# Performance work log

Hardware: AMD Instinct MI355X
Metric: run time of the kernel (lower is better)

Reference implementation:

```python
import jax, jax.numpy as jnp
import numpy as np

N, E, DIN, H, H1, H2, B, DEC = 20000, 320000, 128, 4, 64, 32, 4096, 512


def _seg_softmax(e, seg, n):
    # numerically stable softmax over edges grouped by destination node
    m = jax.ops.segment_max(e, seg, num_segments=n)
    p = jnp.exp(e - m[seg])
    s = jax.ops.segment_sum(p, seg, num_segments=n)
    return p / (s[seg] + 1e-16)


def _prelu(x, a):
    return jnp.where(x >= 0, x, a * x)


def _gat(x, src, dst, n, w, a_src, a_dst, b, concat):
    # PyG GATConv: shared linear, additive attention, leaky_relu(0.2), softmax per dst
    h_, c = a_src.shape
    h = (x @ w).reshape(-1, h_, c)                      # [n, H, C]
    al = jnp.einsum('nhc,hc->nh', h, a_src)[src] + jnp.einsum('nhc,hc->nh', h, a_dst)[dst]
    alpha = _seg_softmax(jax.nn.leaky_relu(al, 0.2), dst, n)  # [e, H]
    out = jax.ops.segment_sum(alpha[..., None] * h[src], dst, num_segments=n)
    out = out.reshape(n, h_ * c) if concat else out.mean(1)
    return out + b


def _gt(x, src, dst, n, wq, bq, wk, bk, wv, bv, ws, bs, heads, concat):
    # PyG TransformerConv: scaled dot-product attention over edges + root skip
    c = wq.shape[1] // heads
    q = (x @ wq + bq).reshape(-1, heads, c)
    k = (x @ wk + bk).reshape(-1, heads, c)
    v = (x @ wv + bv).reshape(-1, heads, c)
    e = (q[dst] * k[src]).sum(-1) / jnp.sqrt(jnp.float32(c))  # [e, heads]
    alpha = _seg_softmax(e, dst, n)
    agg = jax.ops.segment_sum(alpha[..., None] * v[src], dst, num_segments=n)
    agg = agg.reshape(n, heads * c) if concat else agg.mean(1)
    return agg + x @ ws + bs


def _forward(fl, edge_index, idx):
    (x_o, x_a, gat1_w, gat1_asrc, gat1_adst, gat1_b, gat2_w, gat2_asrc, gat2_adst, gat2_b,
     pg1, pg2, gt1_wq, gt1_bq, gt1_wk, gt1_bk, gt1_wv, gt1_bv, gt1_ws, gt1_bs,
     gt2_wq, gt2_bq, gt2_wk, gt2_bk, gt2_wv, gt2_bv, gt2_ws, gt2_bs, pt1, pt2,
     fuse_w, fuse_b, mlp1_w, mlp1_b, disc_w, disc_b,
     fus_w1, fus_b1, fus_w2, fus_b2, fus_w3, fus_b3, adv_w, adv_b) = fl
    n = x_o.shape[0]
    src, dst = edge_index[0], edge_index[1]
    # GATConv adds self loops by default; TransformerConv does not
    loop = jnp.arange(n, dtype=src.dtype)
    src_g = jnp.concatenate([src, loop])
    dst_g = jnp.concatenate([dst, loop])

    def branch_gat(x):
        x1 = _prelu(_gat(x, src_g, dst_g, n, gat1_w, gat1_asrc, gat1_adst, gat1_b, True), pg1)
        return _prelu(_gat(x1, src_g, dst_g, n, gat2_w, gat2_asrc, gat2_adst, gat2_b, False), pg2)

    def branch_gt(x):
        x1 = _prelu(_gt(x, src, dst, n, gt1_wq, gt1_bq, gt1_wk, gt1_bk, gt1_wv, gt1_bv, gt1_ws, gt1_bs, H, True), pt1)
        return _prelu(_gt(x1, src, dst, n, gt2_wq, gt2_bq, gt2_wk, gt2_bk, gt2_wv, gt2_bv, gt2_ws, gt2_bs, 1, False), pt2)

    x2_o = jnp.concatenate([branch_gat(x_o), branch_gt(x_o)], 1) @ fuse_w + fuse_b
    x2_a = jnp.concatenate([branch_gat(x_a), branch_gt(x_a)], 1) @ fuse_w + fuse_b

    def summary(z):
        return jax.nn.sigmoid(z.mean(0)) @ mlp1_w + mlp1_b   # [H2]

    h_os, h_os_a = summary(x2_o), summary(x2_a)

    def disc(cvec, hp, hm):
        # Bilinear(n_h, n_h, 1): sc = h W c^T + b
        s1 = (hp @ disc_w) @ cvec + disc_b[0]
        s2 = (hm @ disc_w) @ cvec + disc_b[0]
        return jnp.stack([s1, s2], 1)                       # [N, 2]

    ret_os = disc(h_os, x2_o, x2_a)
    ret_os_a = disc(h_os_a, x2_a, x2_o)

    # default task_type: direct indexing of node embeddings
    hcat = jnp.concatenate([x2_o[idx[0]], x2_o[idx[1]]], 1)  # [B, 2*H2]
    hh = jax.nn.relu(hcat @ fus_w1 + fus_b1)
    log = hh @ fus_w2 + fus_b2
    log1 = hh @ fus_w3 + fus_b3

    sc1 = (x2_o @ adv_w + adv_b).sum(1)[None, :]
    sc2 = (x2_a @ adv_w + adv_b).sum(1)[None, :]
    logits = jnp.concatenate([sc1, sc2], 1)                  # [1, 2N]
    return (log, ret_os, ret_os_a, x2_o, logits, log1)


_SHAPES = {
    'x_o': (N, DIN), 'x_a': (N, DIN),
    'gat1_w': (DIN, H * H1), 'gat1_asrc': (H, H1), 'gat1_adst': (H, H1), 'gat1_b': (H * H1,),
    'gat2_w': (H * H1, H2), 'gat2_asrc': (1, H2), 'gat2_adst': (1, H2), 'gat2_b': (H2,),
    'pg1': (H * H1,), 'pg2': (H2,),
    'gt1_wq': (DIN, H * H1), 'gt1_bq': (H * H1,), 'gt1_wk': (DIN, H * H1), 'gt1_bk': (H * H1,),
    'gt1_wv': (DIN, H * H1), 'gt1_bv': (H * H1,), 'gt1_ws': (DIN, H * H1), 'gt1_bs': (H * H1,),
    'gt2_wq': (H * H1, H2), 'gt2_bq': (H2,), 'gt2_wk': (H * H1, H2), 'gt2_bk': (H2,),
    'gt2_wv': (H * H1, H2), 'gt2_bv': (H2,), 'gt2_ws': (H * H1, H2), 'gt2_bs': (H2,),
    'pt1': (H * H1,), 'pt2': (H2,),
    'fuse_w': (2 * H2, H2), 'fuse_b': (H2,),
    'mlp1_w': (H2, H2), 'mlp1_b': (H2,),
    'disc_w': (H2, H2), 'disc_b': (1,),
    'fus_w1': (2 * H2, DEC), 'fus_b1': (DEC,), 'fus_w2': (DEC, 2), 'fus_b2': (2,),
    'fus_w3': (DEC, 2), 'fus_b3': (2,),
    'adv_w': (H2, H2), 'adv_b': (H2,),
}


def setup_inputs() -> dict:
    key = jax.random.key(0)
    inp = {}
    for i, (name, shp) in enumerate(_SHAPES.items()):
        inp[name] = jax.random.normal(jax.random.fold_in(key, i), shp, jnp.float32) * 0.05
    inp['edge_index'] = jax.random.randint(jax.random.fold_in(key, 100), (2, E), 0, N, dtype=jnp.int32)
    inp['idx'] = jax.random.randint(jax.random.fold_in(key, 101), (2, B), 0, N, dtype=jnp.int32)
    return inp


def reference(x_o, x_a, gat1_w, gat1_asrc, gat1_adst, gat1_b, gat2_w, gat2_asrc, gat2_adst, gat2_b,
              pg1, pg2, gt1_wq, gt1_bq, gt1_wk, gt1_bk, gt1_wv, gt1_bv, gt1_ws, gt1_bs,
              gt2_wq, gt2_bq, gt2_wk, gt2_bk, gt2_wv, gt2_bv, gt2_ws, gt2_bs, pt1, pt2,
              fuse_w, fuse_b, mlp1_w, mlp1_b, disc_w, disc_b,
              fus_w1, fus_b1, fus_w2, fus_b2, fus_w3, fus_b3, adv_w, adv_b,
              edge_index, idx):
    fl = (x_o, x_a, gat1_w, gat1_asrc, gat1_adst, gat1_b, gat2_w, gat2_asrc, gat2_adst, gat2_b,
          pg1, pg2, gt1_wq, gt1_bq, gt1_wk, gt1_bk, gt1_wv, gt1_bv, gt1_ws, gt1_bs,
          gt2_wq, gt2_bq, gt2_wk, gt2_bk, gt2_wv, gt2_bv, gt2_ws, gt2_bs, pt1, pt2,
          fuse_w, fuse_b, mlp1_w, mlp1_b, disc_w, disc_b,
          fus_w1, fus_b1, fus_w2, fus_b2, fus_w3, fus_b3, adv_w, adv_b)
    return _forward(fl, edge_index, idx)
```

## Files before the change

### kernel.cpp

```cpp
#include <hip/hip_runtime.h>
#include <math.h>

#define NN 20000
#define NE 320000
#define NB 4096

typedef unsigned short u16;
typedef unsigned char u8;
typedef __attribute__((ext_vector_type(8))) short short8;
typedef __attribute__((ext_vector_type(4))) float f32x4;
typedef __attribute__((ext_vector_type(2))) float f32x2;

#define FP8_SCALE 16.0f
#define FP8_INV 0.0625f
#define LOG2E 1.44269504088896341f

__device__ __forceinline__ float b2f(u16 u) {
  unsigned int x = ((unsigned int)u) << 16;
  return __uint_as_float(x);
}
__device__ __forceinline__ u16 f2b(float f) {
  unsigned int x = __float_as_uint(f);
  return (u16)((x + 0x7fffu + ((x >> 16) & 1u)) >> 16);
}
__device__ __forceinline__ float q2f(u8 b) {
  f32x2 v = __builtin_amdgcn_cvt_pk_f32_fp8((int)b, false);
  return v[0];
}
__device__ __forceinline__ void q4(unsigned int u, float* f) {
  f32x2 lo = __builtin_amdgcn_cvt_pk_f32_fp8((int)u, false);
  f32x2 hi = __builtin_amdgcn_cvt_pk_f32_fp8((int)u, true);
  f[0] = lo[0]; f[1] = lo[1]; f[2] = hi[0]; f[3] = hi[1];
}
template <int CTRL>
__device__ __forceinline__ float dppadd(float x) {
  int y = __builtin_amdgcn_update_dpp(0, __float_as_int(x), CTRL, 0xf, 0xf, true);
  return x + __int_as_float(y);
}
__device__ __forceinline__ float red16(float x) {
  x = dppadd<0xB1>(x);
  x = dppadd<0x4E>(x);
  x = dppadd<0x124>(x);
  x = dppadd<0x128>(x);
  return x;
}


__global__ void k_pack1(const float* __restrict__ w0, const float* __restrict__ w1,
                        const float* __restrict__ w2, const float* __restrict__ w3,
                        const float* __restrict__ w4, const float* __restrict__ b1,
                        const float* __restrict__ b2, const float* __restrict__ b3,
                        const float* __restrict__ b4, u16* __restrict__ Wt,
                        float* __restrict__ bp) {
  int t = blockIdx.x * blockDim.x + threadIdx.x;
  if (t < 1280 * 128) {
    int j = t >> 7, k = t & 127;
    int seg = j >> 8, jj = j & 255;
    const float* s = (seg == 0) ? w0 : (seg == 1) ? w1 : (seg == 2) ? w2 : (seg == 3) ? w3 : w4;
    Wt[t] = f2b(s[k * 256 + jj]);
  }
  if (t < 1280) {
    int seg = t >> 8, jj = t & 255;
    bp[t] = (seg == 0) ? 0.0f : (seg == 1) ? b1[jj] : (seg == 2) ? b2[jj] : (seg == 3) ? b3[jj] : b4[jj];
  }
}

__global__ void k_pack2(const float* __restrict__ wq, const float* __restrict__ wk,
                        const float* __restrict__ wv, const float* __restrict__ ws,
                        const float* __restrict__ wg, const float* __restrict__ bq,
                        const float* __restrict__ bk, const float* __restrict__ bv,
                        const float* __restrict__ bs, u16* __restrict__ Wt,
                        float* __restrict__ bp) {
  int t = blockIdx.x * blockDim.x + threadIdx.x;
  if (t < 160 * 256) {
    int j = t >> 8, k = t & 255;
    int seg = j >> 5, jj = j & 31;
    const float* s = (seg == 0) ? wq : (seg == 1) ? wk : (seg == 2) ? wv : (seg == 3) ? ws : wg;
    Wt[t] = f2b(s[k * 32 + jj]);
  }
  if (t < 160) {
    int seg = t >> 5, jj = t & 31;
    bp[t] = (seg == 0) ? bq[jj] : (seg == 1) ? bk[jj] : (seg == 2) ? bv[jj] : (seg == 3) ? bs[jj] : 0.0f;
  }
}

__global__ void k_tobf16x2(const float* __restrict__ xo, const float* __restrict__ xa,
                           u16* __restrict__ bo, u16* __restrict__ ba) {
  int t = blockIdx.x * blockDim.x + threadIdx.x;
  if (t >= 2 * NN * 128) return;
  if (t < NN * 128) bo[t] = f2b(xo[t]);
  else ba[t - NN * 128] = f2b(xa[t - NN * 128]);
}


__global__ void k_hist(const int* __restrict__ dst, int* __restrict__ deg) {
  int t = blockIdx.x * blockDim.x + threadIdx.x;
  if (t < NE) atomicAdd(&deg[dst[t]], 1);
}

__global__ void k_scan20000(const int* __restrict__ deg, int* __restrict__ offs,
                            int* __restrict__ cur) {
  __shared__ int part[1024];
  int t = threadIdx.x;
  int loc[20];
  int s = 0;
#pragma unroll
  for (int i = 0; i < 20; ++i) {
    int idx = t * 20 + i;
    int v = (idx < NN) ? deg[idx] : 0;
    loc[i] = s;
    s += v;
  }
  part[t] = s;
  __syncthreads();
  for (int off = 1; off < 1024; off <<= 1) {
    int v = (t >= off) ? part[t - off] : 0;
    __syncthreads();
    part[t] += v;
    __syncthreads();
  }
  int base = (t > 0) ? part[t - 1] : 0;
#pragma unroll
  for (int i = 0; i < 20; ++i) {
    int idx = t * 20 + i;
    if (idx < NN) {
      offs[idx] = base + loc[i];
      cur[idx] = base + loc[i];
    }
  }
  if (t == 1023) offs[NN] = part[1023];
}

__global__ void k_scatter(const int* __restrict__ src, const int* __restrict__ dst,
                          int* __restrict__ cur, int* __restrict__ esrcs) {
  int t = blockIdx.x * blockDim.x + threadIdx.x;
  if (t >= NE) return;
  int d = dst[t];
  int pos = atomicAdd(&cur[d], 1);
  esrcs[pos] = src[t];
}


template <int LAYER>
__global__ void k_mfma_gemm_s(const u16* __restrict__ A0, const u16* __restrict__ A1,
                              int asel, const u16* __restrict__ Bt,
                              const float* __restrict__ bias, int M, int K, int Nc,
                              u8* __restrict__ G, u16* __restrict__ Cb) {
  const u16* A = (blockIdx.x >= (unsigned)asel) ? A1 : A0;
  int m0 = blockIdx.y * 128, n0 = blockIdx.x * 128;
  int wid = threadIdx.x >> 6, lane = threadIdx.x & 63;
  int mw = m0 + (wid & 1) * 64, nw = n0 + (wid >> 1) * 64;
  int arow = mw + (lane & 15);
  int bcol = nw + (lane & 15);
  int kblk = (lane >> 4) * 8;
  f32x4 acc[4][4] = {};
  const short8 zero8 = {0, 0, 0, 0, 0, 0, 0, 0};
  for (int k0 = 0; k0 < K; k0 += 32) {
    short8 af[4], bf[4];
#pragma unroll
    for (int mf = 0; mf < 4; ++mf) {
      int r = arow + mf * 16;
      if (r > M - 1) r = M - 1;
      af[mf] = *reinterpret_cast<const short8*>(&A[(size_t)r * K + k0 + kblk]);
    }
#pragma unroll
    for (int nf = 0; nf < 4; ++nf) {
      int c = bcol + nf * 16;
      bf[nf] = (c < Nc) ? *reinterpret_cast<const short8*>(&Bt[(size_t)c * K + k0 + kblk])
                        : zero8;
    }
#pragma unroll
    for (int mf = 0; mf < 4; ++mf)
#pragma unroll
      for (int nf = 0; nf < 4; ++nf)
        acc[mf][nf] = __builtin_amdgcn_mfma_f32_16x16x32_bf16(bf[nf], af[mf],
                                                              acc[mf][nf], 0, 0, 0);
  }
  const int CSTR = (LAYER == 1) ? 512 : 64;
  const int GSTR = (LAYER == 1) ? 768 : 96;
#pragma unroll
  for (int mf = 0; mf < 4; ++mf) {
    int row = mw + mf * 16 + (lane & 15);
    if (row >= M) continue;
#pragma unroll
    for (int nf = 0; nf < 4; ++nf) {
      int col0 = nw + nf * 16 + ((lane >> 4) << 2);
      if (col0 >= Nc) continue;
      float4 bs4 = *reinterpret_cast<const float4*>(&bias[col0]);
      float v0 = acc[mf][nf][0] + bs4.x;
      float v1 = acc[mf][nf][1] + bs4.y;
      float v2 = acc[mf][nf][2] + bs4.z;
      float v3 = acc[mf][nf][3] + bs4.w;
      int seg = (LAYER == 1) ? (col0 >> 8) : (col0 >> 5);
      bool tobf = (LAYER == 1) ? (seg == 1 || seg == 4) : (seg == 0 || seg == 3);
      if (tobf) {
        int ccol = (LAYER == 1) ? ((seg == 1) ? col0 - 256 : col0 - 768)
                                : ((seg == 0) ? col0 : col0 - 64);
        ushort4 w4;
        w4.x = f2b(v0); w4.y = f2b(v1); w4.z = f2b(v2); w4.w = f2b(v3);
        *reinterpret_cast<ushort4*>(&Cb[(size_t)row * CSTR + ccol]) = w4;
      } else {
        int gcol = (LAYER == 1) ? ((seg == 0) ? col0 : col0 - 256)
                                : ((seg == 4) ? col0 - 64 : col0 - 32);
        unsigned int p = (unsigned int)__builtin_amdgcn_cvt_pk_fp8_f32(
            v0 * FP8_SCALE, v1 * FP8_SCALE, 0, false);
        p = (unsigned int)__builtin_amdgcn_cvt_pk_fp8_f32(
            v2 * FP8_SCALE, v3 * FP8_SCALE, (int)p, true);
        *reinterpret_cast<unsigned int*>(&G[(size_t)row * GSTR + gcol]) = p;
      }
    }
  }
}


__global__ void k_gat_al8(const u8* __restrict__ h, int stride, int coff,
                          const float* __restrict__ asrc, const float* __restrict__ adst,
                          float* __restrict__ als, float* __restrict__ ald, int total,
                          int heads, int c) {
  int i = blockIdx.x * blockDim.x + threadIdx.x;
  if (i >= total) return;
  int node = i / heads, hd = i - node * heads;
  const u8* hp = h + (size_t)node * stride + coff + hd * c;
  const float* as = asrc + hd * c;
  const float* ad = adst + hd * c;
  float s1 = 0.0f, s2 = 0.0f;
  for (int k = 0; k < c; k += 4) {
    float f[4];
    q4(*reinterpret_cast<const unsigned int*>(&hp[k]), f);
#pragma unroll
    for (int j = 0; j < 4; ++j) {
      s1 = fmaf(f[j], as[k + j], s1);
      s2 = fmaf(f[j], ad[k + j], s2);
    }
  }
  als[i] = s1 * (FP8_INV * LOG2E);
  ald[i] = s2 * (FP8_INV * LOG2E);
}

__global__ void k_agg256_fused(const int* __restrict__ offs, const int* __restrict__ esrcs,
                               const float* __restrict__ als, const float* __restrict__ ald,
                               const u8* __restrict__ G8, const u16* __restrict__ C1b,
                               const float* __restrict__ gbias,
                               const float* __restrict__ pg, const float* __restrict__ pt,
                               u16* __restrict__ outG, u16* __restrict__ outT) {
  __shared__ float part[2][64][10];
  int g = threadIdx.x >> 6;
  int dl = g >> 1, half = g & 1;
  int d = blockIdx.x * 2 + dl;
  int lane = threadIdx.x & 63;
  int head = lane >> 4, c4 = lane << 2;
  ushort4 q4v = *reinterpret_cast<const ushort4*>(&C1b[(size_t)d * 512 + c4]);
  float q0 = b2f(q4v.x), q1 = b2f(q4v.y), q2 = b2f(q4v.z), q3 = b2f(q4v.w);
  float aldd = ald[d * 4 + head];
  float ga0 = 0, ga1 = 0, ga2 = 0, ga3 = 0, gden = 0.0f;
  float ta0 = 0, ta1 = 0, ta2 = 0, ta3 = 0;
  float tden = half ? 0.0f : 1e-16f;
  int bs = offs[d] + half, be = offs[d + 1];
  const float GTC = 0.125f * FP8_INV * LOG2E;
  unsigned int f0 = 0, k0 = 0, v0 = 0, f1 = 0, k1 = 0, v1 = 0;
  float al0 = 0.0f, al1 = 0.0f;
  if (bs < be) {
    int s = esrcs[bs];
    const u8* row = &G8[(size_t)s * 768];
    f0 = *reinterpret_cast<const unsigned int*>(&row[c4]);
    k0 = *reinterpret_cast<const unsigned int*>(&row[256 + c4]);
    v0 = *reinterpret_cast<const unsigned int*>(&row[512 + c4]);
    al0 = als[s * 4 + head];
  }
  if (bs + 2 < be) {
    int s = esrcs[bs + 2];
    const u8* row = &G8[(size_t)s * 768];
    f1 = *reinterpret_cast<const unsigned int*>(&row[c4]);
    k1 = *reinterpret_cast<const unsigned int*>(&row[256 + c4]);
    v1 = *reinterpret_cast<const unsigned int*>(&row[512 + c4]);
    al1 = als[s * 4 + head];
  }
  for (int i = bs; i < be; i += 2) {
    unsigned int f2_ = 0, k2_ = 0, v2_ = 0;
    float al2_ = 0.0f;
    if (i + 4 < be) {
      int s = esrcs[i + 4];
      const u8* row = &G8[(size_t)s * 768];
      f2_ = *reinterpret_cast<const unsigned int*>(&row[c4]);
      k2_ = *reinterpret_cast<const unsigned int*>(&row[256 + c4]);
      v2_ = *reinterpret_cast<const unsigned int*>(&row[512 + c4]);
      al2_ = als[s * 4 + head];
    }
    float kf[4];
    q4(k0, kf);
    float pp = q0 * kf[0];
    pp = fmaf(q1, kf[1], pp);
    pp = fmaf(q2, kf[2], pp);
    pp = fmaf(q3, kf[3], pp);
    pp = red16(pp);
    float pet = exp2f(pp * GTC);
    float v = al0 + aldd;
    float peg = exp2f(v >= 0.0f ? v : 0.2f * v);
    float ff[4], vf[4];
    q4(f0, ff);
    q4(v0, vf);
    ga0 = fmaf(peg, ff[0], ga0);
    ga1 = fmaf(peg, ff[1], ga1);
    ga2 = fmaf(peg, ff[2], ga2);
    ga3 = fmaf(peg, ff[3], ga3);
    gden += peg;
    ta0 = fmaf(pet, vf[0], ta0);
    ta1 = fmaf(pet, vf[1], ta1);
    ta2 = fmaf(pet, vf[2], ta2);
    ta3 = fmaf(pet, vf[3], ta3);
    tden += pet;
    f0 = f1; k0 = k1; v0 = v1; al0 = al1;
    f1 = f2_; k1 = k2_; v1 = v2_; al1 = al2_;
  }
  if (half == 0) {
    float v = als[d * 4 + head] + aldd;
    float pe = exp2f(v >= 0.0f ? v : 0.2f * v);
    float ff[4];
    q4(*reinterpret_cast<const unsigned int*>(&G8[(size_t)d * 768 + c4]), ff);
    ga0 = fmaf(pe, ff[0], ga0);
    ga1 = fmaf(pe, ff[1], ga1);
    ga2 = fmaf(pe, ff[2], ga2);
    ga3 = fmaf(pe, ff[3], ga3);
    gden += pe;
  }
  if (half == 1) {
    float* p = part[dl][lane];
    p[0] = ga0; p[1] = ga1; p[2] = ga2; p[3] = ga3; p[4] = gden;
    p[5] = ta0; p[6] = ta1; p[7] = ta2; p[8] = ta3; p[9] = tden;
  }
  __syncthreads();
  if (half == 1) return;
  const float* p = part[dl][lane];
  ga0 += p[0]; ga1 += p[1]; ga2 += p[2]; ga3 += p[3]; gden += p[4];
  ta0 += p[5]; ta1 += p[6]; ta2 += p[7]; ta3 += p[8]; tden += p[9];
  float ig = FP8_INV / gden, it = FP8_INV / tden;
  float o0 = ga0 * ig + gbias[c4 + 0];
  float o1 = ga1 * ig + gbias[c4 + 1];
  float o2 = ga2 * ig + gbias[c4 + 2];
  float o3 = ga3 * ig + gbias[c4 + 3];
  o0 = o0 >= 0.0f ? o0 : pg[c4 + 0] * o0;
  o1 = o1 >= 0.0f ? o1 : pg[c4 + 1] * o1;
  o2 = o2 >= 0.0f ? o2 : pg[c4 + 2] * o2;
  o3 = o3 >= 0.0f ? o3 : pg[c4 + 3] * o3;
  ushort4 wg4;
  wg4.x = f2b(o0); wg4.y = f2b(o1); wg4.z = f2b(o2); wg4.w = f2b(o3);
  *reinterpret_cast<ushort4*>(&outG[(size_t)d * 256 + c4]) = wg4;
  ushort4 sk = *reinterpret_cast<const ushort4*>(&C1b[(size_t)d * 512 + 256 + c4]);
  float u0 = ta0 * it + b2f(sk.x);
  float u1 = ta1 * it + b2f(sk.y);
  float u2 = ta2 * it + b2f(sk.z);
  float u3 = ta3 * it + b2f(sk.w);
  u0 = u0 >= 0.0f ? u0 : pt[c4 + 0] * u0;
  u1 = u1 >= 0.0f ? u1 : pt[c4 + 1] * u1;
  u2 = u2 >= 0.0f ? u2 : pt[c4 + 2] * u2;
  u3 = u3 >= 0.0f ? u3 : pt[c4 + 3] * u3;
  ushort4 wt4;
  wt4.x = f2b(u0); wt4.y = f2b(u1); wt4.z = f2b(u2); wt4.w = f2b(u3);
  *reinterpret_cast<ushort4*>(&outT[(size_t)d * 256 + c4]) = wt4;
}

__global__ void k_agg32_fuse(const int* __restrict__ offs, const int* __restrict__ esrcs,
                             const float* __restrict__ als, const float* __restrict__ ald,
                             const u8* __restrict__ G28, const u16* __restrict__ C2b,
                             const float* __restrict__ gbias,
                             const float* __restrict__ pg, const float* __restrict__ pt,
                             const float* __restrict__ fw, const float* __restrict__ fb,
                             float* __restrict__ x2out, float* __restrict__ colsum) {
  __shared__ float xgv[8][32], xtv[8][32];
  int g = threadIdx.x >> 5, l = threadIdx.x & 31;
  int d = blockIdx.x * 8 + g;
  float qv = b2f(C2b[(size_t)d * 64 + l]);
  float aldd = ald[d];
  float ga = 0.0f, gden = 0.0f;
  float ta = 0.0f, tden = 1e-16f;
  int b0 = offs[d], b1 = offs[d + 1];
  const float GTC2 = 0.17677669529663687f * FP8_INV * LOG2E;
  u8 kc = 0, vc = 0, hc = 0;
  float alc = 0;
  if (b0 < b1) {
    int sc = esrcs[b0];
    const u8* row = &G28[(size_t)sc * 96];
    kc = row[l]; vc = row[32 + l]; hc = row[64 + l];
    alc = als[sc];
  }
  for (int i = b0; i < b1; ++i) {
    u8 kn = kc, vn = vc, hn = hc;
    float aln = alc;
    if (i + 1 < b1) {
      int sn = esrcs[i + 1];
      const u8* row = &G28[(size_t)sn * 96];
      kn = row[l]; vn = row[32 + l]; hn = row[64 + l];
      aln = als[sn];
    }
    float pp = qv * q2f(kc);
    pp = red16(pp);
    pp += __shfl_xor(pp, 16, 32);
    float pet = exp2f(pp * GTC2);
    float v = alc + aldd;
    float peg = exp2f(v >= 0.0f ? v : 0.2f * v);
    ga = fmaf(peg, q2f(hc), ga);
    gden += peg;
    ta = fmaf(pet, q2f(vc), ta);
    tden += pet;
    kc = kn; vc = vn; hc = hn; alc = aln;
  }
  {
    float v = als[d] + aldd;
    float pe = exp2f(v >= 0.0f ? v : 0.2f * v);
    ga = fmaf(pe, q2f(G28[(size_t)d * 96 + 64 + l]), ga);
    gden += pe;
  }
  float og = ga * FP8_INV / gden + gbias[l];
  og = og >= 0.0f ? og : pg[l] * og;
  float ot = ta * FP8_INV / tden + b2f(C2b[(size_t)d * 64 + 32 + l]);
  ot = ot >= 0.0f ? ot : pt[l] * ot;
  xgv[g][l] = og;
  xtv[g][l] = ot;
  __syncthreads();
  float acc = fb[l];
#pragma unroll
  for (int i = 0; i < 32; ++i) {
    acc = fmaf(xgv[g][i], fw[i * 32 + l], acc);
    acc = fmaf(xtv[g][i], fw[(32 + i) * 32 + l], acc);
  }
  x2out[(size_t)d * 32 + l] = acc;
  __syncthreads();
  xgv[g][l] = acc;
  __syncthreads();
  if (g == 0) {
    float s = acc;
#pragma unroll
    for (int i = 1; i < 8; ++i) s += xgv[i][l];
    atomicAdd(&colsum[(blockIdx.x & 7) * 32 + l], s);
  }
}


__global__ void k_disc_all(const float* __restrict__ x2o, const float* __restrict__ x2a_,
                           const float* __restrict__ cso, const float* __restrict__ csa,
                           const float* __restrict__ mlp_w, const float* __restrict__ mlp_b,
                           const float* __restrict__ disc_w, const float* __restrict__ db,
                           const float* __restrict__ aw, const float* __restrict__ ab,
                           float* __restrict__ ret_os, float* __restrict__ ret_os_a,
                           float* __restrict__ logits) {
  __shared__ float sgv[64], h1s[32], h2s[32], m1[32], m2[32], sadv[33];
  int t = threadIdx.x;
  if (t < 64) {
    int j = t & 31;
    const float* cs = (t < 32) ? cso : csa;
    float m = 0.0f;
#pragma unroll
    for (int i = 0; i < 8; ++i) m += cs[i * 32 + j];
    sgv[t] = 1.0f / (1.0f + expf(-m / (float)NN));
  }
  if (t >= 64 && t < 96) {
    int j = t & 31;
    float s = 0.0f;
#pragma unroll
    for (int i = 0; i < 32; ++i) s += aw[j * 32 + i];
    sadv[j] = s;
  } else if (t == 96) {
    float s = 0.0f;
#pragma unroll
    for (int i = 0; i < 32; ++i) s += ab[i];
    sadv[32] = s;
  }
  __syncthreads();
  if (t < 64) {
    int j = t & 31;
    const float* sg = (t < 32) ? sgv : sgv + 32;
    float acc = mlp_b[j];
#pragma unroll
    for (int i = 0; i < 32; ++i) acc = fmaf(sg[i], mlp_w[i * 32 + j], acc);
    (t < 32 ? h1s : h2s)[j] = acc;
  }
  __syncthreads();
  if (t < 64) {
    int k = t & 31;
    const float* hv = (t < 32) ? h1s : h2s;
    float acc = 0.0f;
#pragma unroll
    for (int i = 0; i < 32; ++i) acc = fmaf(disc_w[k * 32 + i], hv[i], acc);
    (t < 32 ? m1 : m2)[k] = acc;
  }
  __syncthreads();
  int n = blockIdx.x * blockDim.x + t;
  if (n >= NN) return;
  const float* a = x2o + (size_t)n * 32;
  const float* b = x2a_ + (size_t)n * 32;
  float s_oo = 0, s_ao = 0, s_aa = 0, s_oa = 0;
  float lo = sadv[32], la = sadv[32];
#pragma unroll
  for (int i = 0; i < 32; ++i) {
    float v1 = m1[i], v2 = m2[i], av = sadv[i];
    float ai = a[i], bi = b[i];
    s_oo = fmaf(ai, v1, s_oo);
    s_ao = fmaf(bi, v1, s_ao);
    s_aa = fmaf(bi, v2, s_aa);
    s_oa = fmaf(ai, v2, s_oa);
    lo = fmaf(ai, av, lo);
    la = fmaf(bi, av, la);
  }
  float bb = db[0];
  ret_os[n * 2 + 0] = s_oo + bb;
  ret_os[n * 2 + 1] = s_ao + bb;
  ret_os_a[n * 2 + 0] = s_aa + bb;
  ret_os_a[n * 2 + 1] = s_oa + bb;
  logits[n] = lo;
  logits[NN + n] = la;
}

__global__ void k_dec(const float* __restrict__ x2o, const int* __restrict__ idx0,
                      const int* __restrict__ idx1, const float* __restrict__ w1,
                      const float* __restrict__ b1, const float* __restrict__ w2,
                      const float* __restrict__ b2, const float* __restrict__ w3,
                      const float* __restrict__ b3, float* __restrict__ logo,
                      float* __restrict__ log1) {
  __shared__ float hhs[512];
  int bb = blockIdx.x;
  const float* r0 = x2o + (size_t)idx0[bb] * 32;
  const float* r1 = x2o + (size_t)idx1[bb] * 32;
  int t = threadIdx.x;
  for (int n = t; n < 512; n += 256) {
    float acc = b1[n];
#pragma unroll
    for (int i = 0; i < 32; ++i) {
      acc = fmaf(r0[i], w1[i * 512 + n], acc);
      acc = fmaf(r1[i], w1[(32 + i) * 512 + n], acc);
    }
    hhs[n] = fmaxf(acc, 0.0f);
  }
  __syncthreads();
  int g = t >> 6, lane = t & 63;
  const float* ws = (g < 2) ? w2 : w3;
  int jj = g & 1;
  float acc = 0.0f;
#pragma unroll
  for (int k = 0; k < 8; ++k) acc = fmaf(hhs[lane + k * 64], ws[(lane + k * 64) * 2 + jj], acc);
  acc += __shfl_xor(acc, 32);
  acc += __shfl_xor(acc, 16);
  acc += __shfl_xor(acc, 8);
  acc += __shfl_xor(acc, 4);
  acc += __shfl_xor(acc, 2);
  acc += __shfl_xor(acc, 1);
  if (lane == 0) {
    float b = (g < 2) ? b2[jj] : b3[jj];
    ((g < 2) ? logo : log1)[bb * 2 + jj] = acc + b;
  }
}


extern "C" void kernel_launch(void* const* d_in, const int* in_sizes, int n_in,
                              void* d_out, int out_size, void* d_ws, size_t ws_size,
                              hipStream_t stream) {
  const float* x_o = (const float*)d_in[0];
  const float* x_a = (const float*)d_in[1];
  const float* gat1_w = (const float*)d_in[2];
  const float* gat1_asrc = (const float*)d_in[3];
  const float* gat1_adst = (const float*)d_in[4];
  const float* gat1_b = (const float*)d_in[5];
  const float* gat2_w = (const float*)d_in[6];
  const float* gat2_asrc = (const float*)d_in[7];
  const float* gat2_adst = (const float*)d_in[8];
  const float* gat2_b = (const float*)d_in[9];
  const float* pg1 = (const float*)d_in[10];
  const float* pg2 = (const float*)d_in[11];
  const float* gt1_wq = (const float*)d_in[12];
  const float* gt1_bq = (const float*)d_in[13];
  const float* gt1_wk = (const float*)d_in[14];
  const float* gt1_bk = (const float*)d_in[15];
  const float* gt1_wv = (const float*)d_in[16];
  const float* gt1_bv = (const float*)d_in[17];
  const float* gt1_ws = (const float*)d_in[18];
  const float* gt1_bs = (const float*)d_in[19];
  const float* gt2_wq = (const float*)d_in[20];
  const float* gt2_bq = (const float*)d_in[21];
  const float* gt2_wk = (const float*)d_in[22];
  const float* gt2_bk = (const float*)d_in[23];
  const float* gt2_wv = (const float*)d_in[24];
  const float* gt2_bv = (const float*)d_in[25];
  const float* gt2_ws = (const float*)d_in[26];
  const float* gt2_bs = (const float*)d_in[27];
  const float* pt1 = (const float*)d_in[28];
  const float* pt2 = (const float*)d_in[29];
  const float* fuse_w = (const float*)d_in[30];
  const float* fuse_b = (const float*)d_in[31];
  const float* mlp1_w = (const float*)d_in[32];
  const float* mlp1_b = (const float*)d_in[33];
  const float* disc_w = (const float*)d_in[34];
  const float* disc_b = (const float*)d_in[35];
  const float* fus_w1 = (const float*)d_in[36];
  const float* fus_b1 = (const float*)d_in[37];
  const float* fus_w2 = (const float*)d_in[38];
  const float* fus_b2 = (const float*)d_in[39];
  const float* fus_w3 = (const float*)d_in[40];
  const float* fus_b3 = (const float*)d_in[41];
  const float* adv_w = (const float*)d_in[42];
  const float* adv_b = (const float*)d_in[43];
  const int* ei = (const int*)d_in[44];
  const int* idxp = (const int*)d_in[45];
  const int* esrc = ei;
  const int* edst = ei + NE;
  const int* idx0 = idxp;
  const int* idx1 = idxp + NB;

  float* w = (float*)d_ws;
  size_t o = 0;
  u8* G8 = (u8*)(w + o); o += 3840000;
  u16* C1b = (u16*)(w + o); o += 5120000;
  u8* G28 = (u8*)(w + o); o += 480000;
  u16* C2b = (u16*)(w + o); o += 640000;
  u16* bufB = (u16*)(w + o); o += 2560000;
  u16* bufE = (u16*)(w + o); o += 2560000;
  u16* xb_o = (u16*)(w + o); o += 1280000;
  u16* xb_a = (u16*)(w + o); o += 1280000;
  u16* Wt1 = (u16*)(w + o); o += 81920;
  u16* Wt2 = (u16*)(w + o); o += 20480;
  float* bp1 = w + o; o += 1280;
  float* bp2 = w + o; o += 160;
  float* als = w + o; o += NN * 4;
  float* ald = w + o; o += NN * 4;
  float* x2a = w + o; o += NN * 32;
  int* deg = (int*)(w + o); o += NN;
  int* offs = (int*)(w + o); o += NN + 8;
  int* cur = (int*)(w + o); o += NN;
  int* esrcs = (int*)(w + o); o += NE;
  float* colsum_o = w + o; o += 256;
  float* colsum_a = w + o; o += 256;

  float* out = (float*)d_out;
  float* out_log = out;
  float* out_ret = out + 8192;
  float* out_reta = out + 48192;
  float* out_x2o = out + 88192;
  float* out_logit = out + 728192;
  float* out_log1 = out + 768192;

  k_pack1<<<(1280 * 128 + 255) / 256, 256, 0, stream>>>(gat1_w, gt1_wq, gt1_wk, gt1_wv,
                                                        gt1_ws, gt1_bq, gt1_bk, gt1_bv,
                                                        gt1_bs, Wt1, bp1);
  k_pack2<<<(160 * 256 + 255) / 256, 256, 0, stream>>>(gt2_wq, gt2_wk, gt2_wv, gt2_ws,
                                                       gat2_w, gt2_bq, gt2_bk, gt2_bv,
                                                       gt2_bs, Wt2, bp2);
  k_tobf16x2<<<(2 * NN * 128 + 255) / 256, 256, 0, stream>>>(x_o, x_a, xb_o, xb_a);
  hipMemsetAsync(deg, 0, NN * sizeof(int), stream);
  hipMemsetAsync(colsum_o, 0, 512 * sizeof(float), stream);
  k_hist<<<(NE + 255) / 256, 256, 0, stream>>>(edst, deg);
  k_scan20000<<<1, 1024, 0, stream>>>(deg, offs, cur);
  k_scatter<<<(NE + 255) / 256, 256, 0, stream>>>(esrc, edst, cur, esrcs);

  auto branch = [&](const u16* xb, float* x2out, float* colsum) {
    {
      dim3 g(10, (NN + 127) / 128);
      k_mfma_gemm_s<1><<<g, 256, 0, stream>>>(xb, xb, 999, Wt1, bp1, NN, 128, 1280,
                                              G8, C1b);
    }
    k_gat_al8<<<(NN * 4 + 255) / 256, 256, 0, stream>>>(G8, 768, 0, gat1_asrc, gat1_adst,
                                                        als, ald, NN * 4, 4, 64);
    k_agg256_fused<<<NN / 2, 256, 0, stream>>>(offs, esrcs, als, ald, G8, C1b,
                                               gat1_b, pg1, pt1, bufB, bufE);
    {
      dim3 g(2, (NN + 127) / 128);
      k_mfma_gemm_s<2><<<g, 256, 0, stream>>>(bufE, bufB, 1, Wt2, bp2, NN, 256, 160,
                                              G28, C2b);
    }
    k_gat_al8<<<(NN + 255) / 256, 256, 0, stream>>>(G28, 96, 64, gat2_asrc, gat2_adst,
                                                    als, ald, NN, 1, 32);
    k_agg32_fuse<<<NN / 8, 256, 0, stream>>>(offs, esrcs, als, ald, G28, C2b,
                                             gat2_b, pg2, pt2, fuse_w, fuse_b,
                                             x2out, colsum);
  };

  branch(xb_o, out_x2o, colsum_o);
  branch(xb_a, x2a, colsum_a);

  k_disc_all<<<(NN + 255) / 256, 256, 0, stream>>>(out_x2o, x2a, colsum_o, colsum_a,
                                                   mlp1_w, mlp1_b, disc_w, disc_b,
                                                   adv_w, adv_b, out_ret, out_reta,
                                                   out_logit);
  k_dec<<<NB, 256, 0, stream>>>(out_x2o, idx0, idx1, fus_w1, fus_b1, fus_w2, fus_b2,
                                fus_w3, fus_b3, out_log, out_log1);
}
```

Before: 446.8 us.

## Fuse bf16 input conversion and GAT attention logits into GEMM epilogue

Removes the separate fp32-to-bf16 conversion kernel by having the layer-1 GEMM load fp32 inputs and convert them in registers. It also drops both k_gat_al8 launches and computes the per-head source and destination attention logits inside the GEMM epilogue, using full-precision accumulators and cross-lane shuffles. This saves four kernel launches and the global round trips for the bf16 copies and fp8 reloads. In exchange, the GEMM reads twice as many input bytes and converts redundantly across column blocks. The logits now come from unquantized values rather than fp8 values, which slightly changes numerics.

```diff
diff --git a/kernel.cpp b/kernel.cpp
--- a/kernel.cpp
+++ b/kernel.cpp
@@ -43,6 +43,20 @@
   x = dppadd<0x124>(x);
   x = dppadd<0x128>(x);
   return x;
+}
+
+__device__ __forceinline__ short8 lda8(const u16* p) {
+  return *reinterpret_cast<const short8*>(p);
+}
+__device__ __forceinline__ short8 lda8(const float* p) {
+  float4 a = *reinterpret_cast<const float4*>(p);
+  float4 b = *reinterpret_cast<const float4*>(p + 4);
+  short8 r;
+  r[0] = (short)f2b(a.x); r[1] = (short)f2b(a.y);
+  r[2] = (short)f2b(a.z); r[3] = (short)f2b(a.w);
+  r[4] = (short)f2b(b.x); r[5] = (short)f2b(b.y);
+  r[6] = (short)f2b(b.z); r[7] = (short)f2b(b.w);
+  return r;
 }
 
 
@@ -84,14 +98,6 @@
   }
 }
 
-__global__ void k_tobf16x2(const float* __restrict__ xo, const float* __restrict__ xa,
-                           u16* __restrict__ bo, u16* __restrict__ ba) {
-  int t = blockIdx.x * blockDim.x + threadIdx.x;
-  if (t >= 2 * NN * 128) return;
-  if (t < NN * 128) bo[t] = f2b(xo[t]);
-  else ba[t - NN * 128] = f2b(xa[t - NN * 128]);
-}
-
 
 __global__ void k_hist(const int* __restrict__ dst, int* __restrict__ deg) {
   int t = blockIdx.x * blockDim.x + threadIdx.x;
@@ -141,12 +147,15 @@
 }
 
 
-template <int LAYER>
-__global__ void k_mfma_gemm_s(const u16* __restrict__ A0, const u16* __restrict__ A1,
+template <int LAYER, typename TA>
+__global__ void k_mfma_gemm_s(const TA* __restrict__ A0, const TA* __restrict__ A1,
                               int asel, const u16* __restrict__ Bt,
                               const float* __restrict__ bias, int M, int K, int Nc,
-                              u8* __restrict__ G, u16* __restrict__ Cb) {
-  const u16* A = (blockIdx.x >= (unsigned)asel) ? A1 : A0;
+                              u8* __restrict__ G, u16* __restrict__ Cb,
+                              const float* __restrict__ gasrc,
+                              const float* __restrict__ gadst,
+                              float* __restrict__ als, float* __restrict__ ald) {
+  const TA* A = (blockIdx.x >= (unsigned)asel) ? A1 : A0;
   int m0 = blockIdx.y * 128, n0 = blockIdx.x * 128;
   int wid = threadIdx.x >> 6, lane = threadIdx.x & 63;
   int mw = m0 + (wid & 1) * 64, nw = n0 + (wid >> 1) * 64;
@@ -161,7 +170,7 @@
     for (int mf = 0; mf < 4; ++mf) {
       int r = arow + mf * 16;
       if (r > M - 1) r = M - 1;
-      af[mf] = *reinterpret_cast<const short8*>(&A[(size_t)r * K + k0 + kblk]);
+      af[mf] = lda8(&A[(size_t)r * K + k0 + kblk]);
     }
 #pragma unroll
     for (int nf = 0; nf < 4; ++nf) {
@@ -178,10 +187,12 @@
   }
   const int CSTR = (LAYER == 1) ? 512 : 64;
   const int GSTR = (LAYER == 1) ? 768 : 96;
+  bool alwave = (LAYER == 1) ? (n0 < 256) : (nw == 128);
 #pragma unroll
   for (int mf = 0; mf < 4; ++mf) {
     int row = mw + mf * 16 + (lane & 15);
-    if (row >= M) continue;
+    bool rv = row < M;
+    float alsum = 0.0f, aldsum = 0.0f;
 #pragma unroll
     for (int nf = 0; nf < 4; ++nf) {
       int col0 = nw + nf * 16 + ((lane >> 4) << 2);
@@ -191,6 +202,19 @@
       float v1 = acc[mf][nf][1] + bs4.y;
       float v2 = acc[mf][nf][2] + bs4.z;
       float v3 = acc[mf][nf][3] + bs4.w;
+      if (alwave) {
+        if (LAYER == 1) {
+          alsum += v0 * gasrc[col0] + v1 * gasrc[col0 + 1] + v2 * gasrc[col0 + 2] +
+                   v3 * gasrc[col0 + 3];
+          aldsum += v0 * gadst[col0] + v1 * gadst[col0 + 1] + v2 * gadst[col0 + 2] +
+                    v3 * gadst[col0 + 3];
+        } else if (col0 >= 128 && col0 < 160) {
+          int c = col0 - 128;
+          alsum += v0 * gasrc[c] + v1 * gasrc[c + 1] + v2 * gasrc[c + 2] + v3 * gasrc[c + 3];
+          aldsum += v0 * gadst[c] + v1 * gadst[c + 1] + v2 * gadst[c + 2] + v3 * gadst[c + 3];
+        }
+      }
+      if (!rv) continue;
       int seg = (LAYER == 1) ? (col0 >> 8) : (col0 >> 5);
       bool tobf = (LAYER == 1) ? (seg == 1 || seg == 4) : (seg == 0 || seg == 3);
       if (tobf) {
@@ -209,33 +233,25 @@
         *reinterpret_cast<unsigned int*>(&G[(size_t)row * GSTR + gcol]) = p;
       }
     }
-  }
-}
-
-
-__global__ void k_gat_al8(const u8* __restrict__ h, int stride, int coff,
-                          const float* __restrict__ asrc, const float* __restrict__ adst,
-                          float* __restrict__ als, float* __restrict__ ald, int total,
-                          int heads, int c) {
-  int i = blockIdx.x * blockDim.x + threadIdx.x;
-  if (i >= total) return;
-  int node = i / heads, hd = i - node * heads;
-  const u8* hp = h + (size_t)node * stride + coff + hd * c;
-  const float* as = asrc + hd * c;
-  const float* ad = adst + hd * c;
-  float s1 = 0.0f, s2 = 0.0f;
-  for (int k = 0; k < c; k += 4) {
-    float f[4];
-    q4(*reinterpret_cast<const unsigned int*>(&hp[k]), f);
-#pragma unroll
-    for (int j = 0; j < 4; ++j) {
-      s1 = fmaf(f[j], as[k + j], s1);
-      s2 = fmaf(f[j], ad[k + j], s2);
-    }
-  }
-  als[i] = s1 * (FP8_INV * LOG2E);
-  ald[i] = s2 * (FP8_INV * LOG2E);
-}
+    if (alwave) {
+      alsum += __shfl_xor(alsum, 16);
+      alsum += __shfl_xor(alsum, 32);
+      aldsum += __shfl_xor(aldsum, 16);
+      aldsum += __shfl_xor(aldsum, 32);
+      if (lane < 16 && rv) {
+        if (LAYER == 1) {
+          int head = nw >> 6;
+          als[row * 4 + head] = alsum * LOG2E;
+          ald[row * 4 + head] = aldsum * LOG2E;
+        } else {
+          als[row] = alsum * LOG2E;
+          ald[row] = aldsum * LOG2E;
+        }
+      }
+    }
+  }
+}
+
 
 __global__ void k_agg256_fused(const int* __restrict__ offs, const int* __restrict__ esrcs,
                                const float* __restrict__ als, const float* __restrict__ ald,
@@ -612,8 +628,6 @@
   u16* C2b = (u16*)(w + o); o += 640000;
   u16* bufB = (u16*)(w + o); o += 2560000;
   u16* bufE = (u16*)(w + o); o += 2560000;
-  u16* xb_o = (u16*)(w + o); o += 1280000;
-  u16* xb_a = (u16*)(w + o); o += 1280000;
   u16* Wt1 = (u16*)(w + o); o += 81920;
   u16* Wt2 = (u16*)(w + o); o += 20480;
   float* bp1 = w + o; o += 1280;
@@ -642,37 +656,34 @@
   k_pack2<<<(160 * 256 + 255) / 256, 256, 0, stream>>>(gt2_wq, gt2_wk, gt2_wv, gt2_ws,
                                                        gat2_w, gt2_bq, gt2_bk, gt2_bv,
                                                        gt2_bs, Wt2, bp2);
-  k_tobf16x2<<<(2 * NN * 128 + 255) / 256, 256, 0, stream>>>(x_o, x_a, xb_o, xb_a);
   hipMemsetAsync(deg, 0, NN * sizeof(int), stream);
   hipMemsetAsync(colsum_o, 0, 512 * sizeof(float), stream);
   k_hist<<<(NE + 255) / 256, 256, 0, stream>>>(edst, deg);
   k_scan20000<<<1, 1024, 0, stream>>>(deg, offs, cur);
   k_scatter<<<(NE + 255) / 256, 256, 0, stream>>>(esrc, edst, cur, esrcs);
 
-  auto branch = [&](const u16* xb, float* x2out, float* colsum) {
+  auto branch = [&](const float* x, float* x2out, float* colsum) {
     {
       dim3 g(10, (NN + 127) / 128);
-      k_mfma_gemm_s<1><<<g, 256, 0, stream>>>(xb, xb, 999, Wt1, bp1, NN, 128, 1280,
-                                              G8, C1b);
-    }
-    k_gat_al8<<<(NN * 4 + 255) / 256, 256, 0, stream>>>(G8, 768, 0, gat1_asrc, gat1_adst,
-                                                        als, ald, NN * 4, 4, 64);
+      k_mfma_gemm_s<1, float><<<g, 256, 0, stream>>>(x, x, 999, Wt1, bp1, NN, 128, 1280,
+                                                     G8, C1b, gat1_asrc, gat1_adst,
+                                                     als, ald);
+    }
     k_agg256_fused<<<NN / 2, 256, 0, stream>>>(offs, esrcs, als, ald, G8, C1b,
                                                gat1_b, pg1, pt1, bufB, bufE);
     {
       dim3 g(2, (NN + 127) / 128);
-      k_mfma_gemm_s<2><<<g, 256, 0, stream>>>(bufE, bufB, 1, Wt2, bp2, NN, 256, 160,
-                                              G28, C2b);
-    }
-    k_gat_al8<<<(NN + 255) / 256, 256, 0, stream>>>(G28, 96, 64, gat2_asrc, gat2_adst,
-                                                    als, ald, NN, 1, 32);
+      k_mfma_gemm_s<2, u16><<<g, 256, 0, stream>>>(bufE, bufB, 1, Wt2, bp2, NN, 256, 160,
+                                                   G28, C2b, gat2_asrc, gat2_adst,
+                                                   als, ald);
+    }
     k_agg32_fuse<<<NN / 8, 256, 0, stream>>>(offs, esrcs, als, ald, G28, C2b,
                                              gat2_b, pg2, pt2, fuse_w, fuse_b,
                                              x2out, colsum);
   };
 
-  branch(xb_o, out_x2o, colsum_o);
-  branch(xb_a, x2a, colsum_a);
+  branch(x_o, out_x2o, colsum_o);
+  branch(x_a, x2a, colsum_a);
 
   k_disc_all<<<(NN + 255) / 256, 256, 0, stream>>>(out_x2o, x2a, colsum_o, colsum_a,
                                                    mlp1_w, mlp1_b, disc_w, disc_b,
```

After: 473.3 us. 5.9% more time.
